# Performance work log

Measured on AMD Instinct MI355X. Metric: run time of the kernel, lower is better.

The kernel has to match this reference:

```python
import jax, jax.numpy as jnp
import numpy as np
import math

D_MODEL, NHEAD, FACTOR = 1024, 16, 5
EPS = 1e-5


def layer_norm(x, g, b):
    m = jnp.mean(x, -1, keepdims=True)
    v = jnp.mean((x - m) ** 2, -1, keepdims=True)
    return (x - m) / jnp.sqrt(v + EPS) * g + b


def prob_attention(q, k, v, sample_key):
    # Informer ProbSparse causal self-attention. q,k,v: [B,H,L,E]
    B, H, L_Q, E = q.shape
    L_K = k.shape[2]
    U_part = min(FACTOR * int(np.ceil(np.log(L_K))), L_K)  # sampled keys per query
    u = min(FACTOR * int(np.ceil(np.log(L_Q))), L_Q)        # top queries kept
    idx = jax.random.randint(sample_key, (L_Q, U_part), 0, L_K)
    K_sample = k[:, :, idx, :]                               # [B,H,L_Q,U,E]
    QK_sample = jnp.einsum('bhle,bhlue->bhlu', q, K_sample)
    M = QK_sample.max(-1) - QK_sample.sum(-1) / L_K          # sparsity measure
    _, M_top = jax.lax.top_k(M, u)                           # [B,H,u] query indices
    Q_red = jnp.take_along_axis(q, M_top[..., None], axis=2) # [B,H,u,E]
    scores = jnp.einsum('bhue,bhse->bhus', Q_red, k) / math.sqrt(E)
    causal = jnp.arange(L_K)[None, None, None, :] > M_top[..., None]
    scores = jnp.where(causal, -1e9, scores)
    attn = jax.nn.softmax(scores, -1)
    upd = jnp.einsum('bhus,bhsd->bhud', attn, v)             # [B,H,u,E]
    ctx = jnp.cumsum(v, axis=2)                              # causal initial context
    b_i = jnp.arange(B)[:, None, None]
    h_i = jnp.arange(H)[None, :, None]
    return ctx.at[b_i, h_i, M_top].set(upd)


def full_attention(q, k, v):
    # q: [B,L,H,E], k,v: [B,S,H,E]; unmasked cross attention
    E = q.shape[-1]
    scores = jnp.einsum('blhe,bshe->bhls', q, k) / math.sqrt(E)
    A = jax.nn.softmax(scores, -1)
    return jnp.einsum('bhls,bshd->blhd', A, v)


def split_heads(t, B, L):
    return t.reshape(B, L, NHEAD, -1)


def decoder_layer(x, memory, sWq, sbq, sWk, sbk, sWv, sbv, sWo, sbo,
                  cWq, cbq, cWk, cbk, cWv, cbv, cWo, cbo,
                  W1, b1, W2, b2, g1, be1, g2, be2, g3, be3):
    B, L, D = x.shape
    S = memory.shape[1]
    # --- ProbSparse self-attention ---
    q = split_heads(x @ sWq + sbq, B, L).transpose(0, 2, 1, 3)
    k = split_heads(x @ sWk + sbk, B, L).transpose(0, 2, 1, 3)
    v = split_heads(x @ sWv + sbv, B, L).transpose(0, 2, 1, 3)
    ctx = prob_attention(q, k, v, jax.random.key(42))
    sa = ctx.transpose(0, 2, 1, 3).reshape(B, L, D) @ sWo + sbo
    x = layer_norm(x + sa, g1, be1)
    # --- full cross-attention ---
    q = split_heads(x @ cWq + cbq, B, L)
    k = split_heads(memory @ cWk + cbk, B, S)
    v = split_heads(memory @ cWv + cbv, B, S)
    ca = full_attention(q, k, v).reshape(B, L, D) @ cWo + cbo
    x = layer_norm(x + ca, g2, be2)
    # --- conv1d(k=1) FFN == pointwise MLP ---
    y = jax.nn.relu(x @ W1 + b1)
    y = y @ W2 + b2
    return layer_norm(x + y, g3, be3)


def setup_inputs() -> dict:
    key = jax.random.key(0)
    ks = jax.random.split(key, 32)
    D, F = D_MODEL, 4 * D_MODEL
    w = lambda k, sh: (jax.random.normal(k, sh, jnp.float32) * 0.02)
    inp = {
        'x': jax.random.normal(ks[0], (2, 2048, D), jnp.float32),
        'memory': jax.random.normal(ks[1], (2, 2048, D), jnp.float32),
    }
    names = ['sWq', 'sWk', 'sWv', 'sWo', 'cWq', 'cWk', 'cWv', 'cWo']
    for i, n in enumerate(names):
        inp[n] = w(ks[2 + i], (D, D))
        inp[n.replace('W', 'b')] = jnp.zeros((D,), jnp.float32)
    inp['W1'] = w(ks[10], (D, F)); inp['b1'] = jnp.zeros((F,), jnp.float32)
    inp['W2'] = w(ks[11], (F, D)); inp['b2'] = jnp.zeros((D,), jnp.float32)
    for i, n in enumerate(['1', '2', '3']):
        inp['g' + n] = jnp.ones((D,), jnp.float32)
        inp['be' + n] = jnp.zeros((D,), jnp.float32)
    return inp


def reference(x, memory, sWq, sbq, sWk, sbk, sWv, sbv, sWo, sbo,
              cWq, cbq, cWk, cbk, cWv, cbv, cWo, cbo,
              W1, b1, W2, b2, g1, be1, g2, be2, g3, be3):
    return decoder_layer(x, memory, sWq, sbq, sWk, sbk, sWv, sbv, sWo, sbo,
                         cWq, cbq, cWk, cbk, cWv, cbv, cWo, cbo,
                         W1, b1, W2, b2, g1, be1, g2, be2, g3, be3)
```

## Files before the change

### kernel.cpp

```cpp
#include <hip/hip_runtime.h>

static constexpr int BATCH  = 2;
static constexpr int SEQ    = 2048;
static constexpr int DMODEL = 1024;
static constexpr int NHEADS = 16;
static constexpr int EHEAD  = 64;
static constexpr int DFF    = 4096;
static constexpr int NTOP   = 40;

typedef unsigned short u16;
typedef __bf16 bf16x8_t __attribute__((ext_vector_type(8)));
typedef u16    u16x8_t  __attribute__((ext_vector_type(8)));
typedef u16    u16x4_t  __attribute__((ext_vector_type(4)));
typedef float  f32x4_t  __attribute__((ext_vector_type(4)));

static __device__ __forceinline__ u16 f2b(float f) {
  unsigned u = __builtin_bit_cast(unsigned, f);
  unsigned r = u + 0x7FFFu + ((u >> 16) & 1u);
  return (u16)(r >> 16);
}
static __device__ __forceinline__ float b2f(u16 h) {
  unsigned u = ((unsigned)h) << 16;
  return __builtin_bit_cast(float, u);
}
static __device__ __forceinline__ f32x4_t mfma_bf16(u16x8_t a, u16x8_t b, f32x4_t c) {
  return __builtin_amdgcn_mfma_f32_16x16x32_bf16(
      __builtin_bit_cast(bf16x8_t, a), __builtin_bit_cast(bf16x8_t, b), c, 0, 0, 0);
}

#define GLD16(gsrc, ldst)                                                        \
  __builtin_amdgcn_global_load_lds(                                             \
      (const __attribute__((address_space(1))) void*)(gsrc),                    \
      (__attribute__((address_space(3))) void*)(ldst), 16, 0, 0)

static __device__ __forceinline__ void tf2x32(unsigned k0, unsigned k1,
                                              unsigned x0, unsigned x1,
                                              unsigned& o0, unsigned& o1) {
  unsigned ks2 = 0x1BD11BDAu ^ k0 ^ k1;
  x0 += k0; x1 += k1;
#define TFR(r) { x0 += x1; x1 = (x1 << r) | (x1 >> (32 - r)); x1 ^= x0; }
  TFR(13) TFR(15) TFR(26) TFR(6)  x0 += k1;  x1 += ks2 + 1u;
  TFR(17) TFR(29) TFR(16) TFR(24) x0 += ks2; x1 += k0 + 2u;
  TFR(13) TFR(15) TFR(26) TFR(6)  x0 += k0;  x1 += k1 + 3u;
  TFR(17) TFR(29) TFR(16) TFR(24) x0 += k1;  x1 += ks2 + 4u;
  TFR(13) TFR(15) TFR(26) TFR(6)  x0 += ks2; x1 += k0 + 5u;
#undef TFR
  o0 = x0; o1 = x1;
}

__global__ __launch_bounds__(256) void idx_kernel(int* __restrict__ idx) {
  int i = blockIdx.x * 256 + threadIdx.x;
  unsigned c0, c1, o0, o1;
  tf2x32(0u, 42u, 0u, 1u, c0, c1);
  tf2x32(c0, c1, 0u, (unsigned)i, o0, o1);
  idx[i] = (int)((o0 ^ o1) & 2047u);
}

__global__ __launch_bounds__(256)
void wt_kernel(const float* __restrict__ in, u16* __restrict__ outp, int K, int N) {
  __shared__ float t[64][65];
  int k0 = blockIdx.y * 64, n0 = blockIdx.x * 64;
  int c = threadIdx.x & 63, r4 = threadIdx.x >> 6;
#pragma unroll
  for (int i = 0; i < 16; ++i) {
    int r = r4 * 16 + i;
    t[r][c] = in[(size_t)(k0 + r) * N + n0 + c];
  }
  __syncthreads();
#pragma unroll
  for (int i = 0; i < 16; ++i) {
    int r = r4 * 16 + i;
    outp[(size_t)(n0 + r) * K + k0 + c] = f2b(t[c][r]);
  }
}

__global__ __launch_bounds__(256)
void wsplit_kernel(const float* __restrict__ in, u16* __restrict__ oh,
                   u16* __restrict__ ol, int K, int N) {
  __shared__ float t[64][65];
  int k0 = blockIdx.y * 64, n0 = blockIdx.x * 64;
  int c = threadIdx.x & 63, r4 = threadIdx.x >> 6;
#pragma unroll
  for (int i = 0; i < 16; ++i) {
    int r = r4 * 16 + i;
    t[r][c] = in[(size_t)(k0 + r) * N + n0 + c];
  }
  __syncthreads();
#pragma unroll
  for (int i = 0; i < 16; ++i) {
    int r = r4 * 16 + i;
    float f = t[c][r];
    u16 h = f2b(f);
    oh[(size_t)(n0 + r) * K + k0 + c] = h;
    ol[(size_t)(n0 + r) * K + k0 + c] = f2b(f - b2f(h));
  }
}

__global__ __launch_bounds__(256)
void conv_kernel(const float* __restrict__ in, u16* __restrict__ outp) {
  int i = blockIdx.x * 256 + threadIdx.x;
  f32x4_t v = *(const f32x4_t*)(in + (size_t)i * 4);
  u16x4_t o;
  o[0] = f2b(v[0]); o[1] = f2b(v[1]); o[2] = f2b(v[2]); o[3] = f2b(v[3]);
  *(u16x4_t*)(outp + (size_t)i * 4) = o;
}

__global__ __launch_bounds__(256)
void split_kernel(const float* __restrict__ in, u16* __restrict__ oh,
                  u16* __restrict__ ol) {
  int i = blockIdx.x * 256 + threadIdx.x;
  f32x4_t v = *(const f32x4_t*)(in + (size_t)i * 4);
  u16x4_t h, l;
#pragma unroll
  for (int d = 0; d < 4; ++d) {
    u16 hh = f2b(v[d]); h[d] = hh; l[d] = f2b(v[d] - b2f(hh));
  }
  *(u16x4_t*)(oh + (size_t)i * 4) = h;
  *(u16x4_t*)(ol + (size_t)i * 4) = l;
}

__global__ __launch_bounds__(256)
void pack2_kernel(const float* __restrict__ a, const float* __restrict__ b,
                  float* __restrict__ o, int n) {
  int i = blockIdx.x * 256 + threadIdx.x;
  if (i < 2 * n) o[i] = (i < n) ? a[i] : b[i - n];
}

template<int NF>
__global__ __launch_bounds__(256)
void gemm_bf(const u16* __restrict__ A, const u16* __restrict__ Bt,
             const float* __restrict__ bias, float* __restrict__ Cf,
             u16* __restrict__ Cb, int M, int N, int K, int relu) {
  __shared__ __align__(16) u16 sA[2][128 * 32];
  __shared__ __align__(16) u16 sB[2][NF * 32 * 32];
  const int tid = threadIdx.x;
  const int wave = tid >> 6, lane = tid & 63;
  const int m0 = blockIdx.x * 128, n0 = blockIdx.y * (NF * 32);
  const int wr = (wave >> 1) * 64, wc = (wave & 1) * (NF * 16);
  const int lr = lane & 15, kg = lane >> 4;
  const int wv = __builtin_amdgcn_readfirstlane(wave);

  int rowA[2], c8A[2];
#pragma unroll
  for (int rep = 0; rep < 2; ++rep) {
    int P = (rep * 256 + tid) << 4;
    int L = P ^ (((P >> 7) & 3) << 4);
    rowA[rep] = L >> 6; c8A[rep] = (L >> 4) & 3;
  }
  int rowB[NF / 2], c8B[NF / 2];
#pragma unroll
  for (int rep = 0; rep < NF / 2; ++rep) {
    int P = (rep * 256 + tid) << 4;
    int L = P ^ (((P >> 7) & 3) << 4);
    rowB[rep] = L >> 6; c8B[rep] = (L >> 4) & 3;
  }

  f32x4_t acc[4][NF];
#pragma unroll
  for (int i = 0; i < 4; ++i)
#pragma unroll
    for (int j = 0; j < NF; ++j) acc[i][j] = f32x4_t{0.f, 0.f, 0.f, 0.f};

  auto STAGE = [&](int buf, int k0) {
#pragma unroll
    for (int rep = 0; rep < 2; ++rep)
      GLD16(A + (size_t)(m0 + rowA[rep]) * K + k0 + c8A[rep] * 8,
            &sA[buf][(rep * 256 + wv * 64) * 8]);
#pragma unroll
    for (int rep = 0; rep < NF / 2; ++rep)
      GLD16(Bt + (size_t)(n0 + rowB[rep]) * K + k0 + c8B[rep] * 8,
            &sB[buf][(rep * 256 + wv * 64) * 8]);
  };

  const int nk = K >> 5;
  STAGE(0, 0);
  __syncthreads();
  for (int t = 0; t < nk; ++t) {
    const int cur = t & 1;
    if (t + 1 < nk) STAGE(cur ^ 1, (t + 1) << 5);
    u16x8_t a8[4], b8[NF];
#pragma unroll
    for (int mi = 0; mi < 4; ++mi) {
      int La = (wr + mi * 16 + lr) * 64 + kg * 16;
      a8[mi] = *(const u16x8_t*)((const char*)sA[cur] + (La ^ (((La >> 7) & 3) << 4)));
    }
#pragma unroll
    for (int ni = 0; ni < NF; ++ni) {
      int Lb = (wc + ni * 16 + lr) * 64 + kg * 16;
      b8[ni] = *(const u16x8_t*)((const char*)sB[cur] + (Lb ^ (((Lb >> 7) & 3) << 4)));
    }
#pragma unroll
    for (int mi = 0; mi < 4; ++mi)
#pragma unroll
      for (int ni = 0; ni < NF; ++ni)
        acc[mi][ni] = mfma_bf16(a8[mi], b8[ni], acc[mi][ni]);
    __syncthreads();
  }
#pragma unroll
  for (int ni = 0; ni < NF; ++ni) {
    int col = n0 + wc + ni * 16 + lr;
    float bc = bias[col];
#pragma unroll
    for (int mi = 0; mi < 4; ++mi)
#pragma unroll
      for (int r = 0; r < 4; ++r) {
        int row = m0 + wr + mi * 16 + kg * 4 + r;
        float vv = acc[mi][ni][r] + bc;
        if (relu) vv = fmaxf(vv, 0.f);
        if (Cf) Cf[(size_t)row * N + col] = vv;
        if (Cb) Cb[(size_t)row * N + col] = f2b(vv);
      }
  }
}

template<int NF>
__global__ __launch_bounds__(256)
void gemm4_bf(const u16* __restrict__ Ah, const u16* __restrict__ Al,
              const u16* __restrict__ Bh, const u16* __restrict__ Bl,
              const float* __restrict__ bias, float* __restrict__ Cf,
              int M, int N, int K) {
  __shared__ __align__(16) u16 sAh[2][128 * 32];
  __shared__ __align__(16) u16 sAl[2][128 * 32];
  __shared__ __align__(16) u16 sBh[2][NF * 32 * 32];
  __shared__ __align__(16) u16 sBl[2][NF * 32 * 32];
  const int tid = threadIdx.x;
  const int wave = tid >> 6, lane = tid & 63;
  const int m0 = blockIdx.x * 128, n0 = blockIdx.y * (NF * 32);
  const int wr = (wave >> 1) * 64, wc = (wave & 1) * (NF * 16);
  const int lr = lane & 15, kg = lane >> 4;
  const int wv = __builtin_amdgcn_readfirstlane(wave);

  int rowA[2], c8A[2];
#pragma unroll
  for (int rep = 0; rep < 2; ++rep) {
    int P = (rep * 256 + tid) << 4;
    int L = P ^ (((P >> 7) & 3) << 4);
    rowA[rep] = L >> 6; c8A[rep] = (L >> 4) & 3;
  }
  int rowB[NF / 2], c8B[NF / 2];
#pragma unroll
  for (int rep = 0; rep < NF / 2; ++rep) {
    int P = (rep * 256 + tid) << 4;
    int L = P ^ (((P >> 7) & 3) << 4);
    rowB[rep] = L >> 6; c8B[rep] = (L >> 4) & 3;
  }

  f32x4_t acc[4][NF];
#pragma unroll
  for (int i = 0; i < 4; ++i)
#pragma unroll
    for (int j = 0; j < NF; ++j) acc[i][j] = f32x4_t{0.f, 0.f, 0.f, 0.f};

  auto STAGE = [&](int buf, int k0) {
#pragma unroll
    for (int rep = 0; rep < 2; ++rep) {
      GLD16(Ah + (size_t)(m0 + rowA[rep]) * K + k0 + c8A[rep] * 8,
            &sAh[buf][(rep * 256 + wv * 64) * 8]);
      GLD16(Al + (size_t)(m0 + rowA[rep]) * K + k0 + c8A[rep] * 8,
            &sAl[buf][(rep * 256 + wv * 64) * 8]);
    }
#pragma unroll
    for (int rep = 0; rep < NF / 2; ++rep) {
      GLD16(Bh + (size_t)(n0 + rowB[rep]) * K + k0 + c8B[rep] * 8,
            &sBh[buf][(rep * 256 + wv * 64) * 8]);
      GLD16(Bl + (size_t)(n0 + rowB[rep]) * K + k0 + c8B[rep] * 8,
            &sBl[buf][(rep * 256 + wv * 64) * 8]);
    }
  };

  const int nk = K >> 5;
  STAGE(0, 0);
  __syncthreads();
  for (int t = 0; t < nk; ++t) {
    const int cur = t & 1;
    if (t + 1 < nk) STAGE(cur ^ 1, (t + 1) << 5);
    u16x8_t ah[4], al[4], bh[NF], bl[NF];
#pragma unroll
    for (int mi = 0; mi < 4; ++mi) {
      int La = (wr + mi * 16 + lr) * 64 + kg * 16;
      int off = La ^ (((La >> 7) & 3) << 4);
      ah[mi] = *(const u16x8_t*)((const char*)sAh[cur] + off);
      al[mi] = *(const u16x8_t*)((const char*)sAl[cur] + off);
    }
#pragma unroll
    for (int ni = 0; ni < NF; ++ni) {
      int Lb = (wc + ni * 16 + lr) * 64 + kg * 16;
      int off = Lb ^ (((Lb >> 7) & 3) << 4);
      bh[ni] = *(const u16x8_t*)((const char*)sBh[cur] + off);
      bl[ni] = *(const u16x8_t*)((const char*)sBl[cur] + off);
    }
#pragma unroll
    for (int mi = 0; mi < 4; ++mi)
#pragma unroll
      for (int ni = 0; ni < NF; ++ni) {
        acc[mi][ni] = mfma_bf16(ah[mi], bh[ni], acc[mi][ni]);
        acc[mi][ni] = mfma_bf16(ah[mi], bl[ni], acc[mi][ni]);
        acc[mi][ni] = mfma_bf16(al[mi], bh[ni], acc[mi][ni]);
      }
    __syncthreads();
  }
#pragma unroll
  for (int ni = 0; ni < NF; ++ni) {
    int col = n0 + wc + ni * 16 + lr;
    float bc = bias[col];
#pragma unroll
    for (int mi = 0; mi < 4; ++mi)
#pragma unroll
      for (int r = 0; r < 4; ++r) {
        int row = m0 + wr + mi * 16 + kg * 4 + r;
        Cf[(size_t)row * N + col] = acc[mi][ni][r] + bc;
      }
  }
}

__global__ __launch_bounds__(256)
void probM_kernel(const float* __restrict__ qk, const int* __restrict__ idx,
                  float* __restrict__ Mv) {
  int blk = blockIdx.x;
  int xcd = blk & 7, j = blk >> 3;
  int b = xcd >> 2;
  int part = (xcd & 3) * 128 + j;
  int l = part * 4 + (threadIdx.x >> 6);
  int lane = threadIdx.x & 63;
  const float* qrow = qk + ((size_t)b * SEQ + l) * 2048 + lane * 16;
  f32x4_t qv0 = *(const f32x4_t*)(qrow);
  f32x4_t qv1 = *(const f32x4_t*)(qrow + 4);
  f32x4_t qv2 = *(const f32x4_t*)(qrow + 8);
  f32x4_t qv3 = *(const f32x4_t*)(qrow + 12);
  const int* ip = idx + l * NTOP;
  const float* kbase = qk + (size_t)b * SEQ * 2048 + 1024 + lane * 16;
  float mmax = -3.0e38f, msum = 0.f;
#pragma unroll 4
  for (int u = 0; u < NTOP; ++u) {
    int ki = ip[u];
    const float* kr = kbase + (size_t)ki * 2048;
    f32x4_t k0 = *(const f32x4_t*)(kr);
    f32x4_t k1 = *(const f32x4_t*)(kr + 4);
    f32x4_t k2 = *(const f32x4_t*)(kr + 8);
    f32x4_t k3 = *(const f32x4_t*)(kr + 12);
    float p = qv0[0] * k0[0] + qv0[1] * k0[1] + qv0[2] * k0[2] + qv0[3] * k0[3]
            + qv1[0] * k1[0] + qv1[1] * k1[1] + qv1[2] * k1[2] + qv1[3] * k1[3]
            + qv2[0] * k2[0] + qv2[1] * k2[1] + qv2[2] * k2[2] + qv2[3] * k2[3]
            + qv3[0] * k3[0] + qv3[1] * k3[1] + qv3[2] * k3[2] + qv3[3] * k3[3];
    p += __shfl_xor(p, 1);
    p += __shfl_xor(p, 2);
    mmax = fmaxf(mmax, p);
    msum += p;
  }
  if ((lane & 3) == 0) {
    int hh = lane >> 2;
    Mv[((size_t)b * NHEADS + hh) * SEQ + l] = mmax - msum * (1.f / 2048.f);
  }
}

__global__ __launch_bounds__(256)
void topk_kernel(const float* __restrict__ Mv, int* __restrict__ Mtop) {
  int bh = blockIdx.x;
  int tid = threadIdx.x;
  int lane = tid & 63, wv = tid >> 6;
  __shared__ float vals[2048];
  __shared__ float wrv[4];
  __shared__ int wri[4];
  for (int j = tid; j < 2048; j += 256) vals[j] = Mv[bh * 2048 + j];
  __syncthreads();
  for (int it = 0; it < NTOP; ++it) {
    float best = -3.0e38f;
    int bi = 1 << 30;
    for (int j = tid; j < 2048; j += 256) {
      float vv = vals[j];
      if (vv > best) { best = vv; bi = j; }
    }
#pragma unroll
    for (int m = 1; m < 64; m <<= 1) {
      float ov = __shfl_xor(best, m);
      int oi = __shfl_xor(bi, m);
      if (ov > best || (ov == best && oi < bi)) { best = ov; bi = oi; }
    }
    if (lane == 0) { wrv[wv] = best; wri[wv] = bi; }
    __syncthreads();
    if (tid == 0) {
      float bv = wrv[0]; int bbi = wri[0];
#pragma unroll
      for (int t = 1; t < 4; ++t)
        if (wrv[t] > bv || (wrv[t] == bv && wri[t] < bbi)) { bv = wrv[t]; bbi = wri[t]; }
      Mtop[bh * NTOP + it] = bbi;
      vals[bbi] = -3.4e38f;
    }
    __syncthreads();
  }
}

__global__ __launch_bounds__(256)
void kvpack_self(const float* __restrict__ qk, const u16* __restrict__ vbf,
                 u16* __restrict__ kpack, u16* __restrict__ vpack) {
  int bh = blockIdx.x, ch = blockIdx.y;
  int b = bh >> 4, hh = bh & 15;
  int tid = threadIdx.x;
  __shared__ u16 vt[64][80];
#pragma unroll
  for (int rep = 0; rep < 2; ++rep) {
    int u = rep * 256 + tid;
    int key = u >> 3, c = u & 7;
    const float* ksrc = qk + ((size_t)(b * SEQ + ch * 64 + key)) * 2048 + 1024 + hh * 64 + c * 8;
    f32x4_t k0 = *(const f32x4_t*)ksrc;
    f32x4_t k1 = *(const f32x4_t*)(ksrc + 4);
    u16x8_t d;
    d[0] = f2b(k0[0]); d[1] = f2b(k0[1]); d[2] = f2b(k0[2]); d[3] = f2b(k0[3]);
    d[4] = f2b(k1[0]); d[5] = f2b(k1[1]); d[6] = f2b(k1[2]); d[7] = f2b(k1[3]);
    int slot = (key & 3) | (((key >> 3) & 1) << 2);
    *(u16x8_t*)(kpack + ((size_t)bh * SEQ + ch * 64 + key) * 64 + ((c ^ slot) * 8)) = d;
    u16x8_t dv = *(const u16x8_t*)(vbf + ((size_t)(b * SEQ + ch * 64 + key)) * 1024 + hh * 64 + c * 8);
    *(u16x8_t*)(&vt[key][c * 8]) = dv;
  }
  __syncthreads();
#pragma unroll
  for (int rep = 0; rep < 2; ++rep) {
    int u = rep * 256 + tid;
    int e = u >> 3, c = u & 7;
    int kb = (c ^ (e & 7)) * 8;
    u16x8_t d;
#pragma unroll
    for (int j = 0; j < 8; ++j) d[j] = vt[kb + j][e];
    *(u16x8_t*)(vpack + (((size_t)bh * 32 + ch) * 64 + e) * 64 + c * 8) = d;
  }
}

__global__ __launch_bounds__(256)
void probAttn_kernel(const float* __restrict__ qk, const u16* __restrict__ kpack,
                     const u16* __restrict__ vpack, const int* __restrict__ Mtop,
                     float* __restrict__ Opart, float* __restrict__ ml) {
  const int bh = blockIdx.x, b = bh >> 4, hh = bh & 15;
  const int split = blockIdx.y;
  const int tid = threadIdx.x, wave = tid >> 6, lane = tid & 63;
  const int lr = lane & 15, kg = lane >> 4;
  const int wv = __builtin_amdgcn_readfirstlane(wave);
  __shared__ __align__(16) u16 Qs[48 * 64];
  __shared__ __align__(16) u16 Kt[2][64 * 64];
  __shared__ __align__(16) u16 Vt[2][64 * 64];

#pragma unroll
  for (int rep = 0; rep < 3; ++rep) {
    int j = tid + 256 * rep;
    int row = j >> 4, c4 = j & 15;
    int qi = Mtop[bh * NTOP + (row < NTOP ? row : NTOP - 1)];
    f32x4_t v4 = *(const f32x4_t*)(qk + ((size_t)b * SEQ + qi) * 2048 + hh * EHEAD + c4 * 4);
    u16x4_t b4;
    b4[0] = f2b(v4[0] * 0.125f); b4[1] = f2b(v4[1] * 0.125f);
    b4[2] = f2b(v4[2] * 0.125f); b4[3] = f2b(v4[3] * 0.125f);
    *(u16x4_t*)((char*)Qs + ((row * 128 + c4 * 8) ^ ((row & 7) << 4))) = b4;
  }

  const int qtile = (wave < 3) ? wave : 2;
  const int qrow_g = qtile * 16 + lr;
  const int iq = (qrow_g < NTOP) ? Mtop[bh * NTOP + qrow_g] : -1;

  const char* kgl = (const char*)kpack + (size_t)bh * SEQ * 128 + (size_t)split * 4 * 8192;
  const char* vgl = (const char*)vpack + (size_t)bh * 32 * 8192 + (size_t)split * 4 * 8192;
  auto STAGE = [&](int buf, int t) {
    GLD16(kgl + (size_t)t * 8192 + wv * 2048 + lane * 16, (char*)Kt[buf] + wv * 2048);
    GLD16(kgl + (size_t)t * 8192 + wv * 2048 + 1024 + lane * 16, (char*)Kt[buf] + wv * 2048 + 1024);
    GLD16(vgl + (size_t)t * 8192 + wv * 2048 + lane * 16, (char*)Vt[buf] + wv * 2048);
    GLD16(vgl + (size_t)t * 8192 + wv * 2048 + 1024 + lane * 16, (char*)Vt[buf] + wv * 2048 + 1024);
  };

  STAGE(0, 0);
  __syncthreads();

  u16x8_t bq[2];
  {
    int qrow = qtile * 16 + lr;
#pragma unroll
    for (int ks = 0; ks < 2; ++ks)
      bq[ks] = *(u16x8_t*)((char*)Qs + ((qrow * 128 + ks * 64 + kg * 16) ^ ((qrow & 7) << 4)));
  }

  f32x4_t oacc[4];
#pragma unroll
  for (int i = 0; i < 4; ++i) oacc[i] = f32x4_t{0.f, 0.f, 0.f, 0.f};
  float mrun = -3e38f, lrun = 0.f;

  for (int t = 0; t < 4; ++t) {
    const int cur = t & 1;
    if (t + 1 < 4) STAGE(cur ^ 1, t + 1);
    f32x4_t s[4];
#pragma unroll
    for (int i = 0; i < 4; ++i) s[i] = f32x4_t{0.f, 0.f, 0.f, 0.f};
#pragma unroll
    for (int ks = 0; ks < 2; ++ks)
#pragma unroll
      for (int t4 = 0; t4 < 4; ++t4) {
        int arow = ((t4 >> 1) << 5) + ((lr >> 2) << 3) + ((t4 & 1) << 2) + (lr & 3);
        int slot = (arow & 3) | (((arow >> 3) & 1) << 2);
        int off = (arow << 7) + (ks << 6) + (kg << 4);
        u16x8_t ak = *(const u16x8_t*)((const char*)Kt[cur] + (off ^ (slot << 4)));
        s[t4] = mfma_bf16(ak, bq[ks], s[t4]);
      }
    const int kb0 = split * 256 + t * 64;
#pragma unroll
    for (int t4 = 0; t4 < 4; ++t4)
#pragma unroll
      for (int r = 0; r < 4; ++r) {
        int gkey = kb0 + ((t4 >> 1) << 5) + (kg << 3) + ((t4 & 1) << 2) + r;
        if (gkey > iq) s[t4][r] = -1e9f;
      }
    float mx = s[0][0];
#pragma unroll
    for (int t4 = 0; t4 < 4; ++t4)
#pragma unroll
      for (int r = 0; r < 4; ++r) mx = fmaxf(mx, s[t4][r]);
    mx = fmaxf(mx, __shfl_xor(mx, 16));
    mx = fmaxf(mx, __shfl_xor(mx, 32));
    float mnew = fmaxf(mrun, mx);
    float a = __expf(mrun - mnew);
    float sum = 0.f;
#pragma unroll
    for (int t4 = 0; t4 < 4; ++t4)
#pragma unroll
      for (int r = 0; r < 4; ++r) {
        float p = __expf(s[t4][r] - mnew);
        s[t4][r] = p; sum += p;
      }
    sum += __shfl_xor(sum, 16);
    sum += __shfl_xor(sum, 32);
    lrun = lrun * a + sum;
    mrun = mnew;
    float ar[4];
#pragma unroll
    for (int r = 0; r < 4; ++r) ar[r] = __shfl(a, kg * 4 + r);
#pragma unroll
    for (int ne = 0; ne < 4; ++ne)
#pragma unroll
      for (int r = 0; r < 4; ++r) oacc[ne][r] *= ar[r];
#pragma unroll
    for (int ks2 = 0; ks2 < 2; ++ks2) {
      u16x8_t pa;
#pragma unroll
      for (int j = 0; j < 4; ++j) {
        pa[j] = f2b(s[2 * ks2][j]);
        pa[4 + j] = f2b(s[2 * ks2 + 1][j]);
      }
#pragma unroll
      for (int ne = 0; ne < 4; ++ne) {
        int e = ne * 16 + lr;
        int off = (e << 7) + (ks2 << 6) + (kg << 4);
        u16x8_t bv = *(const u16x8_t*)((const char*)Vt[cur] + (off ^ ((e & 7) << 4)));
        oacc[ne] = mfma_bf16(pa, bv, oacc[ne]);
      }
    }
    __syncthreads();
  }

  if (wave < 3) {
    float* ob = Opart + (((size_t)(bh * 8 + split)) * 48 + qtile * 16) * 64;
#pragma unroll
    for (int ne = 0; ne < 4; ++ne)
#pragma unroll
      for (int r = 0; r < 4; ++r)
        ob[(size_t)(kg * 4 + r) * 64 + ne * 16 + lr] = oacc[ne][r];
    if (kg == 0) {
      size_t mb = (((size_t)(bh * 8 + split)) * 48 + qtile * 16 + lr) * 2;
      ml[mb + 0] = mrun;
      ml[mb + 1] = lrun;
    }
  }
}

__global__ __launch_bounds__(64)
void probCombine_kernel(const float* __restrict__ Opart, const float* __restrict__ ml,
                        const int* __restrict__ Mtop, u16* __restrict__ ctxb) {
  int bh = blockIdx.x / NTOP, q = blockIdx.x % NTOP;
  int e = threadIdx.x;
  int b = bh >> 4, hh = bh & 15;
  float ms[8], ls[8];
  float mstar = -3.0e38f;
#pragma unroll
  for (int s = 0; s < 8; ++s) {
    size_t mb = (((size_t)(bh * 8 + s)) * 48 + q) * 2;
    ms[s] = ml[mb + 0];
    ls[s] = ml[mb + 1];
    mstar = fmaxf(mstar, ms[s]);
  }
  float lstar = 0.f, acc = 0.f;
#pragma unroll
  for (int s = 0; s < 8; ++s) {
    float w = __expf(ms[s] - mstar);
    lstar += w * ls[s];
    acc += w * Opart[(((size_t)(bh * 8 + s)) * 48 + q) * 64 + e];
  }
  int row = Mtop[bh * NTOP + q];
  ctxb[((size_t)b * SEQ + row) * DMODEL + hh * EHEAD + e] = f2b(acc / lstar);
}

__global__ __launch_bounds__(64)
void scan1_kernel(const u16* __restrict__ v, float* __restrict__ ctx,
                  float* __restrict__ csum) {
  int bh = blockIdx.x, c = blockIdx.y;
  int b = bh >> 4, hh = bh & 15, e = threadIdx.x;
  size_t base = ((size_t)b * SEQ + c * 128) * DMODEL + hh * EHEAD + e;
  float run = 0.f;
  for (int i = 0; i < 128; ++i) {
    run += b2f(v[base + (size_t)i * DMODEL]);
    ctx[base + (size_t)i * DMODEL] = run;
  }
  csum[(bh * 16 + c) * 64 + e] = run;
}

__global__ __launch_bounds__(64)
void scan2_kernel(const float* __restrict__ csum, const float* __restrict__ ctxf,
                  u16* __restrict__ ctxb) {
  int bh = blockIdx.x, c = blockIdx.y;
  int b = bh >> 4, hh = bh & 15, e = threadIdx.x;
  float off = 0.f;
  for (int cc = 0; cc < c; ++cc) off += csum[(bh * 16 + cc) * 64 + e];
  size_t base = ((size_t)b * SEQ + c * 128) * DMODEL + hh * EHEAD + e;
  for (int i = 0; i < 128; ++i)
    ctxb[base + (size_t)i * DMODEL] = f2b(ctxf[base + (size_t)i * DMODEL] + off);
}

__global__ __launch_bounds__(256)
void kvpack_kernel(const u16* __restrict__ kv, u16* __restrict__ kpack,
                   u16* __restrict__ vpack) {
  int bh = blockIdx.x, ch = blockIdx.y;
  int b = bh >> 4, hh = bh & 15;
  int tid = threadIdx.x;
  __shared__ u16 vt[64][80];
#pragma unroll
  for (int rep = 0; rep < 2; ++rep) {
    int u = rep * 256 + tid;
    int key = u >> 3, c = u & 7;
    u16x8_t d = *(const u16x8_t*)(kv + ((size_t)(b * SEQ + ch * 64 + key)) * 2048 + hh * 64 + c * 8);
    int slot = (key & 3) | (((key >> 3) & 1) << 2);
    *(u16x8_t*)(kpack + ((size_t)bh * SEQ + ch * 64 + key) * 64 + ((c ^ slot) * 8)) = d;
    u16x8_t dv = *(const u16x8_t*)(kv + ((size_t)(b * SEQ + ch * 64 + key)) * 2048 + 1024 + hh * 64 + c * 8);
    *(u16x8_t*)(&vt[key][c * 8]) = dv;
  }
  __syncthreads();
#pragma unroll
  for (int rep = 0; rep < 2; ++rep) {
    int u = rep * 256 + tid;
    int e = u >> 3, c = u & 7;
    int kb = (c ^ (e & 7)) * 8;
    u16x8_t d;
#pragma unroll
    for (int j = 0; j < 8; ++j) d[j] = vt[kb + j][e];
    *(u16x8_t*)(vpack + (((size_t)bh * 32 + ch) * 64 + e) * 64 + c * 8) = d;
  }
}

__global__ __launch_bounds__(512)
void cross_attn_kernel(const float* __restrict__ q2, const u16* __restrict__ kpack,
                       const u16* __restrict__ vpack, u16* __restrict__ cab) {
  const int bh = blockIdx.x, b = bh >> 4, hh = bh & 15;
  const int qt0 = blockIdx.y * 128;
  const int tid = threadIdx.x, wave = tid >> 6, lane = tid & 63;
  const int lr = lane & 15, kg = lane >> 4;
  const int wv = __builtin_amdgcn_readfirstlane(wave);
  __shared__ __align__(16) u16 Qs[128 * 64];
  __shared__ __align__(16) u16 Kt[2][64 * 64];
  __shared__ __align__(16) u16 Vt[2][64 * 64];

#pragma unroll
  for (int i = 0; i < 4; ++i) {
    int j = tid + 512 * i;
    int row = j >> 4, c4 = j & 15;
    f32x4_t v4 = *(const f32x4_t*)(q2 + ((size_t)b * SEQ + qt0 + row) * DMODEL + hh * EHEAD + c4 * 4);
    u16x4_t b4;
    b4[0] = f2b(v4[0] * 0.125f); b4[1] = f2b(v4[1] * 0.125f);
    b4[2] = f2b(v4[2] * 0.125f); b4[3] = f2b(v4[3] * 0.125f);
    *(u16x4_t*)((char*)Qs + ((row * 128 + c4 * 8) ^ ((row & 7) << 4))) = b4;
  }

  const char* kgl = (const char*)kpack + (size_t)bh * SEQ * 128;
  const char* vgl = (const char*)vpack + (size_t)bh * 32 * 8192;
  auto STAGE = [&](int buf, int t) {
    GLD16(kgl + (size_t)t * 8192 + wv * 1024 + lane * 16, (char*)Kt[buf] + wv * 1024);
    GLD16(vgl + (size_t)t * 8192 + wv * 1024 + lane * 16, (char*)Vt[buf] + wv * 1024);
  };

  STAGE(0, 0);
  __syncthreads();

  u16x8_t bq[2];
  {
    int qrow = wave * 16 + lr;
#pragma unroll
    for (int ks = 0; ks < 2; ++ks)
      bq[ks] = *(u16x8_t*)((char*)Qs + ((qrow * 128 + ks * 64 + kg * 16) ^ ((qrow & 7) << 4)));
  }

  f32x4_t oacc[4];
#pragma unroll
  for (int i = 0; i < 4; ++i) oacc[i] = f32x4_t{0.f, 0.f, 0.f, 0.f};
  float mrun = -3e38f, lrun = 0.f;

  for (int t = 0; t < 32; ++t) {
    const int cur = t & 1;
    if (t + 1 < 32) STAGE(cur ^ 1, t + 1);
    f32x4_t s[4];
#pragma unroll
    for (int i = 0; i < 4; ++i) s[i] = f32x4_t{0.f, 0.f, 0.f, 0.f};
#pragma unroll
    for (int ks = 0; ks < 2; ++ks)
#pragma unroll
      for (int t4 = 0; t4 < 4; ++t4) {
        int arow = ((t4 >> 1) << 5) + ((lr >> 2) << 3) + ((t4 & 1) << 2) + (lr & 3);
        int slot = (arow & 3) | (((arow >> 3) & 1) << 2);
        int off = (arow << 7) + (ks << 6) + (kg << 4);
        u16x8_t ak = *(const u16x8_t*)((const char*)Kt[cur] + (off ^ (slot << 4)));
        s[t4] = mfma_bf16(ak, bq[ks], s[t4]);
      }
    float mx = s[0][0];
#pragma unroll
    for (int t4 = 0; t4 < 4; ++t4)
#pragma unroll
      for (int r = 0; r < 4; ++r) mx = fmaxf(mx, s[t4][r]);
    mx = fmaxf(mx, __shfl_xor(mx, 16));
    mx = fmaxf(mx, __shfl_xor(mx, 32));
    float mnew = fmaxf(mrun, mx);
    float a = __expf(mrun - mnew);
    float sum = 0.f;
#pragma unroll
    for (int t4 = 0; t4 < 4; ++t4)
#pragma unroll
      for (int r = 0; r < 4; ++r) {
        float p = __expf(s[t4][r] - mnew);
        s[t4][r] = p; sum += p;
      }
    sum += __shfl_xor(sum, 16);
    sum += __shfl_xor(sum, 32);
    lrun = lrun * a + sum;
    mrun = mnew;
    float ar[4];
#pragma unroll
    for (int r = 0; r < 4; ++r) ar[r] = __shfl(a, kg * 4 + r);
#pragma unroll
    for (int ne = 0; ne < 4; ++ne)
#pragma unroll
      for (int r = 0; r < 4; ++r) oacc[ne][r] *= ar[r];
#pragma unroll
    for (int ks2 = 0; ks2 < 2; ++ks2) {
      u16x8_t pa;
#pragma unroll
      for (int j = 0; j < 4; ++j) {
        pa[j] = f2b(s[2 * ks2][j]);
        pa[4 + j] = f2b(s[2 * ks2 + 1][j]);
      }
#pragma unroll
      for (int ne = 0; ne < 4; ++ne) {
        int e = ne * 16 + lr;
        int off = (e << 7) + (ks2 << 6) + (kg << 4);
        u16x8_t bv = *(const u16x8_t*)((const char*)Vt[cur] + (off ^ ((e & 7) << 4)));
        oacc[ne] = mfma_bf16(pa, bv, oacc[ne]);
      }
    }
    __syncthreads();
  }

  float lr4[4];
#pragma unroll
  for (int r = 0; r < 4; ++r) lr4[r] = __shfl(lrun, kg * 4 + r);
#pragma unroll
  for (int ne = 0; ne < 4; ++ne)
#pragma unroll
    for (int r = 0; r < 4; ++r) {
      int row = qt0 + wave * 16 + kg * 4 + r;
      int col = hh * EHEAD + ne * 16 + lr;
      cab[((size_t)b * SEQ + row) * DMODEL + col] = f2b(oacc[ne][r] / lr4[r]);
    }
}

__global__ __launch_bounds__(256)
void ln_kernel(const float* __restrict__ x, const float* __restrict__ r,
               const float* __restrict__ g, const float* __restrict__ be,
               float* __restrict__ outf, u16* __restrict__ outb) {
  int row = blockIdx.x, tid = threadIdx.x;
  size_t base = (size_t)row * DMODEL;
  float v[4];
  float s = 0.f, sq = 0.f;
#pragma unroll
  for (int i = 0; i < 4; ++i) {
    int c = tid + i * 256;
    float t = x[base + c] + r[base + c];
    v[i] = t; s += t; sq += t * t;
  }
  __shared__ float rs[256], rq[256];
  rs[tid] = s; rq[tid] = sq;
  __syncthreads();
  for (int st = 128; st > 0; st >>= 1) {
    if (tid < st) { rs[tid] += rs[tid + st]; rq[tid] += rq[tid + st]; }
    __syncthreads();
  }
  float mean = rs[0] * (1.f / DMODEL);
  float var = rq[0] * (1.f / DMODEL) - mean * mean;
  float rstd = rsqrtf(var + 1e-5f);
#pragma unroll
  for (int i = 0; i < 4; ++i) {
    int c = tid + i * 256;
    float o = (v[i] - mean) * rstd * g[c] + be[c];
    if (outf) outf[base + c] = o;
    if (outb) outb[base + c] = f2b(o);
  }
}

static inline void gemm(const u16* A, const u16* Bt, const float* bias, float* Cf,
                        u16* Cb, int M, int N, int K, int relu, hipStream_t s,
                        int big = 0) {
  if (big)
    gemm_bf<4><<<dim3(M / 128, N / 128), 256, 0, s>>>(A, Bt, bias, Cf, Cb, M, N, K, relu);
  else
    gemm_bf<2><<<dim3(M / 128, N / 64), 256, 0, s>>>(A, Bt, bias, Cf, Cb, M, N, K, relu);
}
static inline void gemm4(const u16* Ah, const u16* Al, const u16* Bh, const u16* Bl,
                         const float* bias, float* Cf, int M, int N, int K, hipStream_t s) {
  gemm4_bf<4><<<dim3(M / 128, N / 128), 256, 0, s>>>(Ah, Al, Bh, Bl, bias, Cf, M, N, K);
}

extern "C" void kernel_launch(void* const* d_in, const int* in_sizes, int n_in,
                              void* d_out, int out_size, void* d_ws, size_t ws_size,
                              hipStream_t stream) {
  const float* x   = (const float*)d_in[0];
  const float* mem = (const float*)d_in[1];
  const float* sWq = (const float*)d_in[2];  const float* sbq = (const float*)d_in[3];
  const float* sWk = (const float*)d_in[4];  const float* sbk = (const float*)d_in[5];
  const float* sWv = (const float*)d_in[6];  const float* sbv = (const float*)d_in[7];
  const float* sWo = (const float*)d_in[8];  const float* sbo = (const float*)d_in[9];
  const float* cWq = (const float*)d_in[10]; const float* cbq = (const float*)d_in[11];
  const float* cWk = (const float*)d_in[12]; const float* cbk = (const float*)d_in[13];
  const float* cWv = (const float*)d_in[14]; const float* cbv = (const float*)d_in[15];
  const float* cWo = (const float*)d_in[16]; const float* cbo = (const float*)d_in[17];
  const float* W1  = (const float*)d_in[18]; const float* b1  = (const float*)d_in[19];
  const float* W2  = (const float*)d_in[20]; const float* b2  = (const float*)d_in[21];
  const float* g1  = (const float*)d_in[22]; const float* be1 = (const float*)d_in[23];
  const float* g2  = (const float*)d_in[24]; const float* be2 = (const float*)d_in[25];
  const float* g3  = (const float*)d_in[26]; const float* be3 = (const float*)d_in[27];
  float* outp = (float*)d_out;
  char* ws = (char*)d_ws;
  const size_t MB = 1ull << 20;

  int*   idx    = (int*)(ws);
  float* Mv     = (float*)(ws + 0x60000);
  int*   Mtop   = (int*)(ws + 0xA0000);
  float* csum   = (float*)(ws + 0x100000);
  float* biasqk = (float*)(ws + 0x120000);
  float* cbkv   = (float*)(ws + 0x122000);

  u16* WqkhT = (u16*)(ws + 2 * MB);
  u16* WqklT = (u16*)(ws + 6 * MB);
  u16* sWvT  = (u16*)(ws + 10 * MB);
  u16* sWoT  = (u16*)(ws + 12 * MB);
  u16* cWqT  = (u16*)(ws + 14 * MB);
  u16* cWkvT = (u16*)(ws + 16 * MB);
  u16* cWoT  = (u16*)(ws + 20 * MB);
  u16* W1T   = (u16*)(ws + 22 * MB);
  u16* W2T   = (u16*)(ws + 30 * MB);

  u16* xh   = (u16*)(ws + 38 * MB);
  u16* xl   = (u16*)(ws + 46 * MB);
  u16* memb = (u16*)(ws + 54 * MB);

  float* qk    = (float*)(ws + 62 * MB);
  u16*   vbf   = (u16*)(ws + 94 * MB);
  u16*   kpks  = (u16*)(ws + 102 * MB);
  u16*   vpks  = (u16*)(ws + 46 * MB);
  float* Opart = (float*)(ws + 110 * MB);
  float* mlbuf = (float*)(ws + 113 * MB);
  float* ctxf  = (float*)(ws + 62 * MB);
  u16*   ctxb  = (u16*)(ws + 78 * MB);
  float* sa    = (float*)(ws + 94 * MB);
  float* x1    = (float*)(ws + 62 * MB);
  u16*   x1b   = (u16*)(ws + 78 * MB);
  float* q2    = (float*)(ws + 94 * MB);
  u16*   kv2b  = (u16*)(ws + 38 * MB);
  u16*   kpk   = (u16*)(ws + 54 * MB);
  u16*   vpk   = (u16*)(ws + 110 * MB);
  u16*   cab   = (u16*)(ws + 38 * MB);
  float* ca2   = (float*)(ws + 94 * MB);
  float* x2    = (float*)(ws + 38 * MB);
  u16*   x2b   = (u16*)(ws + 54 * MB);
  u16*   hbb   = (u16*)(ws + 62 * MB);
  float* yb    = (float*)(ws + 94 * MB);

  const int MROWS = BATCH * SEQ;

  idx_kernel<<<320, 256, 0, stream>>>(idx);
  wsplit_kernel<<<dim3(16, 16), 256, 0, stream>>>(sWq, WqkhT, WqklT, 1024, 1024);
  wsplit_kernel<<<dim3(16, 16), 256, 0, stream>>>(sWk, WqkhT + 1024 * 1024, WqklT + 1024 * 1024, 1024, 1024);
  wt_kernel<<<dim3(16, 16), 256, 0, stream>>>(sWv, sWvT, 1024, 1024);
  wt_kernel<<<dim3(16, 16), 256, 0, stream>>>(sWo, sWoT, 1024, 1024);
  wt_kernel<<<dim3(16, 16), 256, 0, stream>>>(cWq, cWqT, 1024, 1024);
  wt_kernel<<<dim3(16, 16), 256, 0, stream>>>(cWk, cWkvT, 1024, 1024);
  wt_kernel<<<dim3(16, 16), 256, 0, stream>>>(cWv, cWkvT + 1024 * 1024, 1024, 1024);
  wt_kernel<<<dim3(16, 16), 256, 0, stream>>>(cWo, cWoT, 1024, 1024);
  wt_kernel<<<dim3(64, 16), 256, 0, stream>>>(W1, W1T, 1024, 4096);
  wt_kernel<<<dim3(16, 64), 256, 0, stream>>>(W2, W2T, 4096, 1024);
  split_kernel<<<4096, 256, 0, stream>>>(x, xh, xl);
  conv_kernel<<<4096, 256, 0, stream>>>(mem, memb);
  pack2_kernel<<<8, 256, 0, stream>>>(sbq, sbk, biasqk, 1024);
  pack2_kernel<<<8, 256, 0, stream>>>(cbk, cbv, cbkv, 1024);

  gemm4(xh, xl, WqkhT, WqklT, biasqk, qk, MROWS, 2048, DMODEL, stream);
  gemm(xh, sWvT, sbv, nullptr, vbf, MROWS, DMODEL, DMODEL, 0, stream);
  probM_kernel<<<BATCH * SEQ / 4, 256, 0, stream>>>(qk, idx, Mv);
  topk_kernel<<<BATCH * NHEADS, 256, 0, stream>>>(Mv, Mtop);
  kvpack_self<<<dim3(BATCH * NHEADS, SEQ / 64), 256, 0, stream>>>(qk, vbf, kpks, vpks);
  probAttn_kernel<<<dim3(BATCH * NHEADS, 8), 256, 0, stream>>>(qk, kpks, vpks, Mtop, Opart, mlbuf);
  scan1_kernel<<<dim3(BATCH * NHEADS, 16), 64, 0, stream>>>(vbf, ctxf, csum);
  scan2_kernel<<<dim3(BATCH * NHEADS, 16), 64, 0, stream>>>(csum, ctxf, ctxb);
  probCombine_kernel<<<BATCH * NHEADS * NTOP, 64, 0, stream>>>(Opart, mlbuf, Mtop, ctxb);
  gemm(ctxb, sWoT, sbo, sa, nullptr, MROWS, DMODEL, DMODEL, 0, stream);
  ln_kernel<<<MROWS, 256, 0, stream>>>(x, sa, g1, be1, x1, x1b);

  gemm(x1b, cWqT, cbq, q2, nullptr, MROWS, DMODEL, DMODEL, 0, stream);
  gemm(memb, cWkvT, cbkv, nullptr, kv2b, MROWS, 2048, DMODEL, 0, stream, 1);
  kvpack_kernel<<<dim3(BATCH * NHEADS, SEQ / 64), 256, 0, stream>>>(kv2b, kpk, vpk);
  cross_attn_kernel<<<dim3(BATCH * NHEADS, SEQ / 128), 512, 0, stream>>>(q2, kpk, vpk, cab);
  gemm(cab, cWoT, cbo, ca2, nullptr, MROWS, DMODEL, DMODEL, 0, stream);
  ln_kernel<<<MROWS, 256, 0, stream>>>(x1, ca2, g2, be2, x2, x2b);

  gemm(x2b, W1T, b1, nullptr, hbb, MROWS, DFF, DMODEL, 1, stream, 1);
  gemm(hbb, W2T, b2, yb, nullptr, MROWS, DMODEL, DFF, 0, stream);
  ln_kernel<<<MROWS, 256, 0, stream>>>(x2, yb, g3, be3, outp, nullptr);
}
```

Measured before the change: 586.7 us.

## Batch weight/input prep kernels, fuse cumsum scan, register-resident topk, localized probM

Merges the eight weight-transpose launches into two batched kernels, and the input conversion and bias packing kernels into single launches, to cut launch overhead. The two-pass cumsum scan becomes one kernel with 1024 threads per head that keeps chunk sums in shared memory, which drops the fp32 intermediate buffer and its round trip. Top-k now holds its values in registers instead of scanning shared memory on every iteration. probM walks the sampled keys in four passes over index windows to improve cache locality, which adds redundant index checks. The single-block-per-head scan launches only 32 blocks, so parallelism is low.

```diff
diff --git a/kernel.cpp b/kernel.cpp
--- a/kernel.cpp
+++ b/kernel.cpp
@@ -74,16 +74,40 @@
   }
 }
 
-__global__ __launch_bounds__(256)
-void wsplit_kernel(const float* __restrict__ in, u16* __restrict__ oh,
-                   u16* __restrict__ ol, int K, int N) {
+struct Ptr6 { const float* s[6]; u16* d[6]; };
+__global__ __launch_bounds__(256)
+void wt6_kernel(Ptr6 p) {
+  const float* in = p.s[blockIdx.z];
+  u16* outp = p.d[blockIdx.z];
   __shared__ float t[64][65];
   int k0 = blockIdx.y * 64, n0 = blockIdx.x * 64;
   int c = threadIdx.x & 63, r4 = threadIdx.x >> 6;
 #pragma unroll
   for (int i = 0; i < 16; ++i) {
     int r = r4 * 16 + i;
-    t[r][c] = in[(size_t)(k0 + r) * N + n0 + c];
+    t[r][c] = in[(size_t)(k0 + r) * 1024 + n0 + c];
+  }
+  __syncthreads();
+#pragma unroll
+  for (int i = 0; i < 16; ++i) {
+    int r = r4 * 16 + i;
+    outp[(size_t)(n0 + r) * 1024 + k0 + c] = f2b(t[c][r]);
+  }
+}
+
+struct Ptr2 { const float* s[2]; u16* dh[2]; u16* dl[2]; };
+__global__ __launch_bounds__(256)
+void wsplit2_kernel(Ptr2 p) {
+  const float* in = p.s[blockIdx.z];
+  u16* oh = p.dh[blockIdx.z];
+  u16* ol = p.dl[blockIdx.z];
+  __shared__ float t[64][65];
+  int k0 = blockIdx.y * 64, n0 = blockIdx.x * 64;
+  int c = threadIdx.x & 63, r4 = threadIdx.x >> 6;
+#pragma unroll
+  for (int i = 0; i < 16; ++i) {
+    int r = r4 * 16 + i;
+    t[r][c] = in[(size_t)(k0 + r) * 1024 + n0 + c];
   }
   __syncthreads();
 #pragma unroll
@@ -91,39 +115,44 @@
     int r = r4 * 16 + i;
     float f = t[c][r];
     u16 h = f2b(f);
-    oh[(size_t)(n0 + r) * K + k0 + c] = h;
-    ol[(size_t)(n0 + r) * K + k0 + c] = f2b(f - b2f(h));
-  }
-}
-
-__global__ __launch_bounds__(256)
-void conv_kernel(const float* __restrict__ in, u16* __restrict__ outp) {
+    oh[(size_t)(n0 + r) * 1024 + k0 + c] = h;
+    ol[(size_t)(n0 + r) * 1024 + k0 + c] = f2b(f - b2f(h));
+  }
+}
+
+__global__ __launch_bounds__(256)
+void prep_inputs(const float* __restrict__ x, u16* __restrict__ xh,
+                 u16* __restrict__ xl, const float* __restrict__ mem,
+                 u16* __restrict__ memb) {
+  int blk = blockIdx.x;
+  if (blk < 4096) {
+    int i = blk * 256 + threadIdx.x;
+    f32x4_t v = *(const f32x4_t*)(x + (size_t)i * 4);
+    u16x4_t h, l;
+#pragma unroll
+    for (int d = 0; d < 4; ++d) {
+      u16 hh = f2b(v[d]); h[d] = hh; l[d] = f2b(v[d] - b2f(hh));
+    }
+    *(u16x4_t*)(xh + (size_t)i * 4) = h;
+    *(u16x4_t*)(xl + (size_t)i * 4) = l;
+  } else {
+    int i = (blk - 4096) * 256 + threadIdx.x;
+    f32x4_t v = *(const f32x4_t*)(mem + (size_t)i * 4);
+    u16x4_t o;
+    o[0] = f2b(v[0]); o[1] = f2b(v[1]); o[2] = f2b(v[2]); o[3] = f2b(v[3]);
+    *(u16x4_t*)(memb + (size_t)i * 4) = o;
+  }
+}
+
+__global__ __launch_bounds__(256)
+void pack4_kernel(const float* __restrict__ a0, const float* __restrict__ a1,
+                  float* __restrict__ o0, const float* __restrict__ b0,
+                  const float* __restrict__ b1, float* __restrict__ o1) {
   int i = blockIdx.x * 256 + threadIdx.x;
-  f32x4_t v = *(const f32x4_t*)(in + (size_t)i * 4);
-  u16x4_t o;
-  o[0] = f2b(v[0]); o[1] = f2b(v[1]); o[2] = f2b(v[2]); o[3] = f2b(v[3]);
-  *(u16x4_t*)(outp + (size_t)i * 4) = o;
-}
-
-__global__ __launch_bounds__(256)
-void split_kernel(const float* __restrict__ in, u16* __restrict__ oh,
-                  u16* __restrict__ ol) {
-  int i = blockIdx.x * 256 + threadIdx.x;
-  f32x4_t v = *(const f32x4_t*)(in + (size_t)i * 4);
-  u16x4_t h, l;
-#pragma unroll
-  for (int d = 0; d < 4; ++d) {
-    u16 hh = f2b(v[d]); h[d] = hh; l[d] = f2b(v[d] - b2f(hh));
-  }
-  *(u16x4_t*)(oh + (size_t)i * 4) = h;
-  *(u16x4_t*)(ol + (size_t)i * 4) = l;
-}
-
-__global__ __launch_bounds__(256)
-void pack2_kernel(const float* __restrict__ a, const float* __restrict__ b,
-                  float* __restrict__ o, int n) {
-  int i = blockIdx.x * 256 + threadIdx.x;
-  if (i < 2 * n) o[i] = (i < n) ? a[i] : b[i - n];
+  if (i < 1024) o0[i] = a0[i];
+  else if (i < 2048) o0[i] = a1[i - 1024];
+  else if (i < 3072) o1[i - 2048] = b0[i - 2048];
+  else o1[i - 2048] = b1[i - 3072];
 }
 
 template<int NF>
@@ -330,22 +359,27 @@
   const int* ip = idx + l * NTOP;
   const float* kbase = qk + (size_t)b * SEQ * 2048 + 1024 + lane * 16;
   float mmax = -3.0e38f, msum = 0.f;
+  for (int pass = 0; pass < 4; ++pass) {
+    int lo = pass << 9;
 #pragma unroll 4
-  for (int u = 0; u < NTOP; ++u) {
-    int ki = ip[u];
-    const float* kr = kbase + (size_t)ki * 2048;
-    f32x4_t k0 = *(const f32x4_t*)(kr);
-    f32x4_t k1 = *(const f32x4_t*)(kr + 4);
-    f32x4_t k2 = *(const f32x4_t*)(kr + 8);
-    f32x4_t k3 = *(const f32x4_t*)(kr + 12);
-    float p = qv0[0] * k0[0] + qv0[1] * k0[1] + qv0[2] * k0[2] + qv0[3] * k0[3]
-            + qv1[0] * k1[0] + qv1[1] * k1[1] + qv1[2] * k1[2] + qv1[3] * k1[3]
-            + qv2[0] * k2[0] + qv2[1] * k2[1] + qv2[2] * k2[2] + qv2[3] * k2[3]
-            + qv3[0] * k3[0] + qv3[1] * k3[1] + qv3[2] * k3[2] + qv3[3] * k3[3];
-    p += __shfl_xor(p, 1);
-    p += __shfl_xor(p, 2);
-    mmax = fmaxf(mmax, p);
-    msum += p;
+    for (int u = 0; u < NTOP; ++u) {
+      int ki = ip[u];
+      if ((unsigned)(ki - lo) < 512u) {
+        const float* kr = kbase + (size_t)ki * 2048;
+        f32x4_t k0 = *(const f32x4_t*)(kr);
+        f32x4_t k1 = *(const f32x4_t*)(kr + 4);
+        f32x4_t k2 = *(const f32x4_t*)(kr + 8);
+        f32x4_t k3 = *(const f32x4_t*)(kr + 12);
+        float p = qv0[0] * k0[0] + qv0[1] * k0[1] + qv0[2] * k0[2] + qv0[3] * k0[3]
+                + qv1[0] * k1[0] + qv1[1] * k1[1] + qv1[2] * k1[2] + qv1[3] * k1[3]
+                + qv2[0] * k2[0] + qv2[1] * k2[1] + qv2[2] * k2[2] + qv2[3] * k2[3]
+                + qv3[0] * k3[0] + qv3[1] * k3[1] + qv3[2] * k3[2] + qv3[3] * k3[3];
+        p += __shfl_xor(p, 1);
+        p += __shfl_xor(p, 2);
+        mmax = fmaxf(mmax, p);
+        msum += p;
+      }
+    }
   }
   if ((lane & 3) == 0) {
     int hh = lane >> 2;
@@ -358,18 +392,19 @@
   int bh = blockIdx.x;
   int tid = threadIdx.x;
   int lane = tid & 63, wv = tid >> 6;
-  __shared__ float vals[2048];
+  float v8[8];
+#pragma unroll
+  for (int j = 0; j < 8; ++j) v8[j] = Mv[bh * 2048 + j * 256 + tid];
   __shared__ float wrv[4];
   __shared__ int wri[4];
-  for (int j = tid; j < 2048; j += 256) vals[j] = Mv[bh * 2048 + j];
-  __syncthreads();
+  __shared__ int winner;
   for (int it = 0; it < NTOP; ++it) {
-    float best = -3.0e38f;
-    int bi = 1 << 30;
-    for (int j = tid; j < 2048; j += 256) {
-      float vv = vals[j];
-      if (vv > best) { best = vv; bi = j; }
-    }
+    float best = v8[0];
+    int bj = 0;
+#pragma unroll
+    for (int j = 1; j < 8; ++j)
+      if (v8[j] > best) { best = v8[j]; bj = j; }
+    int bi = bj * 256 + tid;
 #pragma unroll
     for (int m = 1; m < 64; m <<= 1) {
       float ov = __shfl_xor(best, m);
@@ -384,9 +419,13 @@
       for (int t = 1; t < 4; ++t)
         if (wrv[t] > bv || (wrv[t] == bv && wri[t] < bbi)) { bv = wrv[t]; bbi = wri[t]; }
       Mtop[bh * NTOP + it] = bbi;
-      vals[bbi] = -3.4e38f;
+      winner = bbi;
     }
     __syncthreads();
+    int w = winner;
+#pragma unroll
+    for (int j = 0; j < 8; ++j)
+      if ((w >> 8) == j && (w & 255) == tid) v8[j] = -3.4e38f;
   }
 }
 
@@ -591,30 +630,24 @@
   ctxb[((size_t)b * SEQ + row) * DMODEL + hh * EHEAD + e] = f2b(acc / lstar);
 }
 
-__global__ __launch_bounds__(64)
-void scan1_kernel(const u16* __restrict__ v, float* __restrict__ ctx,
-                  float* __restrict__ csum) {
-  int bh = blockIdx.x, c = blockIdx.y;
-  int b = bh >> 4, hh = bh & 15, e = threadIdx.x;
-  size_t base = ((size_t)b * SEQ + c * 128) * DMODEL + hh * EHEAD + e;
+__global__ __launch_bounds__(1024)
+void scan_kernel(const u16* __restrict__ v, u16* __restrict__ ctxb) {
+  int bh = blockIdx.x;
+  int b = bh >> 4, hh = bh & 15;
+  int e = threadIdx.x & 63, ch = threadIdx.x >> 6;
+  size_t base = ((size_t)b * SEQ + ch * 128) * DMODEL + hh * EHEAD + e;
   float run = 0.f;
+  for (int i = 0; i < 128; ++i) run += b2f(v[base + (size_t)i * DMODEL]);
+  __shared__ float cs[16][64];
+  cs[ch][e] = run;
+  __syncthreads();
+  float off = 0.f;
+  for (int cc = 0; cc < ch; ++cc) off += cs[cc][e];
+  run = off;
   for (int i = 0; i < 128; ++i) {
     run += b2f(v[base + (size_t)i * DMODEL]);
-    ctx[base + (size_t)i * DMODEL] = run;
-  }
-  csum[(bh * 16 + c) * 64 + e] = run;
-}
-
-__global__ __launch_bounds__(64)
-void scan2_kernel(const float* __restrict__ csum, const float* __restrict__ ctxf,
-                  u16* __restrict__ ctxb) {
-  int bh = blockIdx.x, c = blockIdx.y;
-  int b = bh >> 4, hh = bh & 15, e = threadIdx.x;
-  float off = 0.f;
-  for (int cc = 0; cc < c; ++cc) off += csum[(bh * 16 + cc) * 64 + e];
-  size_t base = ((size_t)b * SEQ + c * 128) * DMODEL + hh * EHEAD + e;
-  for (int i = 0; i < 128; ++i)
-    ctxb[base + (size_t)i * DMODEL] = f2b(ctxf[base + (size_t)i * DMODEL] + off);
+    ctxb[base + (size_t)i * DMODEL] = f2b(run);
+  }
 }
 
 __global__ __launch_bounds__(256)
@@ -840,7 +873,6 @@
   int*   idx    = (int*)(ws);
   float* Mv     = (float*)(ws + 0x60000);
   int*   Mtop   = (int*)(ws + 0xA0000);
-  float* csum   = (float*)(ws + 0x100000);
   float* biasqk = (float*)(ws + 0x120000);
   float* cbkv   = (float*)(ws + 0x122000);
 
@@ -864,7 +896,6 @@
   u16*   vpks  = (u16*)(ws + 46 * MB);
   float* Opart = (float*)(ws + 110 * MB);
   float* mlbuf = (float*)(ws + 113 * MB);
-  float* ctxf  = (float*)(ws + 62 * MB);
   u16*   ctxb  = (u16*)(ws + 78 * MB);
   float* sa    = (float*)(ws + 94 * MB);
   float* x1    = (float*)(ws + 62 * MB);
@@ -883,20 +914,24 @@
   const int MROWS = BATCH * SEQ;
 
   idx_kernel<<<320, 256, 0, stream>>>(idx);
-  wsplit_kernel<<<dim3(16, 16), 256, 0, stream>>>(sWq, WqkhT, WqklT, 1024, 1024);
-  wsplit_kernel<<<dim3(16, 16), 256, 0, stream>>>(sWk, WqkhT + 1024 * 1024, WqklT + 1024 * 1024, 1024, 1024);
-  wt_kernel<<<dim3(16, 16), 256, 0, stream>>>(sWv, sWvT, 1024, 1024);
-  wt_kernel<<<dim3(16, 16), 256, 0, stream>>>(sWo, sWoT, 1024, 1024);
-  wt_kernel<<<dim3(16, 16), 256, 0, stream>>>(cWq, cWqT, 1024, 1024);
-  wt_kernel<<<dim3(16, 16), 256, 0, stream>>>(cWk, cWkvT, 1024, 1024);
-  wt_kernel<<<dim3(16, 16), 256, 0, stream>>>(cWv, cWkvT + 1024 * 1024, 1024, 1024);
-  wt_kernel<<<dim3(16, 16), 256, 0, stream>>>(cWo, cWoT, 1024, 1024);
+  {
+    Ptr2 p2;
+    p2.s[0] = sWq; p2.dh[0] = WqkhT;              p2.dl[0] = WqklT;
+    p2.s[1] = sWk; p2.dh[1] = WqkhT + 1024*1024;  p2.dl[1] = WqklT + 1024*1024;
+    wsplit2_kernel<<<dim3(16, 16, 2), 256, 0, stream>>>(p2);
+    Ptr6 p6;
+    p6.s[0] = sWv; p6.d[0] = sWvT;
+    p6.s[1] = sWo; p6.d[1] = sWoT;
+    p6.s[2] = cWq; p6.d[2] = cWqT;
+    p6.s[3] = cWk; p6.d[3] = cWkvT;
+    p6.s[4] = cWv; p6.d[4] = cWkvT + 1024*1024;
+    p6.s[5] = cWo; p6.d[5] = cWoT;
+    wt6_kernel<<<dim3(16, 16, 6), 256, 0, stream>>>(p6);
+  }
   wt_kernel<<<dim3(64, 16), 256, 0, stream>>>(W1, W1T, 1024, 4096);
   wt_kernel<<<dim3(16, 64), 256, 0, stream>>>(W2, W2T, 4096, 1024);
-  split_kernel<<<4096, 256, 0, stream>>>(x, xh, xl);
-  conv_kernel<<<4096, 256, 0, stream>>>(mem, memb);
-  pack2_kernel<<<8, 256, 0, stream>>>(sbq, sbk, biasqk, 1024);
-  pack2_kernel<<<8, 256, 0, stream>>>(cbk, cbv, cbkv, 1024);
+  prep_inputs<<<8192, 256, 0, stream>>>(x, xh, xl, mem, memb);
+  pack4_kernel<<<16, 256, 0, stream>>>(sbq, sbk, biasqk, cbk, cbv, cbkv);
 
   gemm4(xh, xl, WqkhT, WqklT, biasqk, qk, MROWS, 2048, DMODEL, stream);
   gemm(xh, sWvT, sbv, nullptr, vbf, MROWS, DMODEL, DMODEL, 0, stream);
@@ -904,8 +939,7 @@
   topk_kernel<<<BATCH * NHEADS, 256, 0, stream>>>(Mv, Mtop);
   kvpack_self<<<dim3(BATCH * NHEADS, SEQ / 64), 256, 0, stream>>>(qk, vbf, kpks, vpks);
   probAttn_kernel<<<dim3(BATCH * NHEADS, 8), 256, 0, stream>>>(qk, kpks, vpks, Mtop, Opart, mlbuf);
-  scan1_kernel<<<dim3(BATCH * NHEADS, 16), 64, 0, stream>>>(vbf, ctxf, csum);
-  scan2_kernel<<<dim3(BATCH * NHEADS, 16), 64, 0, stream>>>(csum, ctxf, ctxb);
+  scan_kernel<<<BATCH * NHEADS, 1024, 0, stream>>>(vbf, ctxb);
   probCombine_kernel<<<BATCH * NHEADS * NTOP, 64, 0, stream>>>(Opart, mlbuf, Mtop, ctxb);
   gemm(ctxb, sWoT, sbo, sa, nullptr, MROWS, DMODEL, DMODEL, 0, stream);
   ln_kernel<<<MROWS, 256, 0, stream>>>(x, sa, g1, be1, x1, x1b);
```

Result: faster. 551.5 us (-6.0%).
